# Kernel tuning notes

Measured on AMD Instinct MI355X. Metric: run time of the kernel, lower is better.

## Reference

```python
import jax, jax.numpy as jnp
import numpy as np

# Coarse-to-fine lossless 3D segmentation (Seg3dLossless), batch=1, C=1.
RES = [17, 33, 65, 129]          # odd resolutions, stride (RF-1)/(R-1) is integral
RF = RES[-1]
B_MIN, B_MAX = -1.0, 1.0
BAL = 0.5                        # balance_value
N_CONFLICT_ITERS = 2             # fixed unroll of the data-dependent while-loop


def _mlp(pts, w1, b1, w2, b2, w3, b3):
    # query_func: occupancy MLP on normalized (x,y,z) points -> [N]
    h = jax.nn.relu(pts @ w1 + b1)
    h = jax.nn.relu(h @ w2 + b2)
    return jax.nn.sigmoid(h @ w3 + b3)[..., 0]


def _eval_grid(R, w1, b1, w2, b2, w3, b3):
    # batch_eval with align_corners=False: coords2D = (coord + 0.5)/RF, mapped to [B_MIN,B_MAX]
    s = (RF - 1) // (R - 1)
    c = jnp.arange(R, dtype=jnp.float32) * s                 # final-res integer coords
    p = (c + 0.5) / RF * (B_MAX - B_MIN) + B_MIN
    zz, yy, xx = jnp.meshgrid(p, p, p, indexing='ij')        # [D,H,W]
    pts = jnp.stack([xx, yy, zz], axis=-1).reshape(-1, 3)    # (x,y,z) order
    return _mlp(pts, w1, b1, w2, b2, w3, b3).reshape(R, R, R)


def _resize(x, R):
    # trilinear, align_corners=True: out index j -> in coord j*(in-1)/(out-1)
    c = jnp.linspace(0.0, x.shape[0] - 1.0, R)
    zz, yy, xx = jnp.meshgrid(c, c, c, indexing='ij')
    return jax.scipy.ndimage.map_coordinates(x, [zz, yy, xx], order=1, mode='nearest')


def _dilate(m):
    # smooth_conv3x3 (mean filter) followed by >0 == 3x3x3 binary dilation
    f = jax.lax.reduce_window(m.astype(jnp.float32), 0.0, jax.lax.max,
                              (3, 3, 3), (1, 1, 1), 'SAME')
    return f > 0.0


def setup_inputs() -> dict:
    key = jax.random.key(0)
    k1, k2, k3 = jax.random.split(key, 3)
    H = 64
    return {
        'w1': jax.random.normal(k1, (3, H), jnp.float32) * 0.8,
        'b1': jnp.zeros((H,), jnp.float32),
        'w2': jax.random.normal(k2, (H, H), jnp.float32) * (1.0 / np.sqrt(H)),
        'b2': jnp.zeros((H,), jnp.float32),
        'w3': jax.random.normal(k3, (H, 1), jnp.float32) * (1.0 / np.sqrt(H)),
        'b3': jnp.zeros((1,), jnp.float32),
    }


def reference(w1, b1, w2, b2, w3, b3):
    params = (w1, b1, w2, b2, w3, b3)
    # level 0: dense eval on the coarse grid
    occ = _eval_grid(RES[0], *params)                        # [R0,R0,R0]
    s0 = (RF - 1) // (RES[0] - 1)
    calculated = jnp.zeros((RF, RF, RF), bool).at[::s0, ::s0, ::s0].set(True)

    for R in RES[1:]:
        s = (RF - 1) // (R - 1)
        valid = _resize((occ > BAL).astype(jnp.float32), R)  # no-grad mask path
        occ_i = _resize(occ, R)                              # differentiable interp
        boundary = _dilate((valid > 0.0) & (valid < 1.0))
        calc_l = calculated[::s, ::s, ::s]
        boundary = boundary & (~calc_l)                      # skip already-evaluated voxels
        occ_true = _eval_grid(R, *params)                    # query_func at this level
        occ = jnp.where(boundary, occ_true, occ_i)           # scatter of occupancys_topk
        calc_l = calc_l | boundary
        # conflict resolution: re-query 3^3 neighbors of sign-flip voxels
        conflict = boundary & ((occ_i - BAL) * (occ_true - BAL) < 0.0)
        for _ in range(N_CONFLICT_ITERS):
            nbr = _dilate(conflict) & (~calc_l)
            occ_prev = occ
            occ = jnp.where(nbr, occ_true, occ)
            calc_l = calc_l | nbr
            conflict = nbr & ((occ_prev - BAL) * (occ_true - BAL) < 0.0)
        calculated = calculated.at[::s, ::s, ::s].set(calc_l)

    return occ[None, None]                                   # (1, 1, D, H, W)
```

## Files before the change

### kernel.cpp

```cpp
#include <hip/hip_runtime.h>

#define HH 64

static __global__ void k_prep_w2t(const float* __restrict__ w2, float* __restrict__ w2t){
  int t = blockIdx.x * 256 + threadIdx.x;
  w2t[t] = w2[(t & 63) * HH + (t >> 6)];
}

__device__ __forceinline__ void mlp_pair(
    const float* __restrict__ sw1,
    const float* __restrict__ sw2t,
    const float* __restrict__ b2, const float* __restrict__ w3,
    const float* __restrict__ b3,
    float xA, float yA, float zA, float xB, float yB, float zB,
    float& outA, float& outB)
{
  const int ibase = ((threadIdx.x & 63) >> 5) * 32;
  float h1a[32], h1b[32];
  #pragma unroll
  for (int k = 0; k < 32; k += 4){
    const float4 wx = *(const float4*)&sw1[      ibase + k];
    const float4 wy = *(const float4*)&sw1[ 64 + ibase + k];
    const float4 wz = *(const float4*)&sw1[128 + ibase + k];
    const float4 bb = *(const float4*)&sw1[192 + ibase + k];
    h1a[k+0] = fmaxf(fmaf(xA,wx.x,fmaf(yA,wy.x,fmaf(zA,wz.x,bb.x))),0.f);
    h1a[k+1] = fmaxf(fmaf(xA,wx.y,fmaf(yA,wy.y,fmaf(zA,wz.y,bb.y))),0.f);
    h1a[k+2] = fmaxf(fmaf(xA,wx.z,fmaf(yA,wy.z,fmaf(zA,wz.z,bb.z))),0.f);
    h1a[k+3] = fmaxf(fmaf(xA,wx.w,fmaf(yA,wy.w,fmaf(zA,wz.w,bb.w))),0.f);
    h1b[k+0] = fmaxf(fmaf(xB,wx.x,fmaf(yB,wy.x,fmaf(zB,wz.x,bb.x))),0.f);
    h1b[k+1] = fmaxf(fmaf(xB,wx.y,fmaf(yB,wy.y,fmaf(zB,wz.y,bb.y))),0.f);
    h1b[k+2] = fmaxf(fmaf(xB,wx.z,fmaf(yB,wy.z,fmaf(zB,wz.z,bb.z))),0.f);
    h1b[k+3] = fmaxf(fmaf(xB,wx.w,fmaf(yB,wy.w,fmaf(zB,wz.w,bb.w))),0.f);
  }
  float oa = b3[0], ob = oa;
  #pragma unroll 1
  for (int j = 0; j < HH; ++j){
    const float4* wrow = (const float4*)&sw2t[j*HH + ibase];
    float a0 = 0.f, a1 = 0.f, c0 = 0.f, c1 = 0.f;
    #pragma unroll
    for (int q = 0; q < 8; q += 2){
      const float4 w0 = wrow[q];
      const float4 w1q = wrow[q+1];
      a0 = fmaf(h1a[4*q+0], w0.x, a0);
      a0 = fmaf(h1a[4*q+1], w0.y, a0);
      a0 = fmaf(h1a[4*q+2], w0.z, a0);
      a0 = fmaf(h1a[4*q+3], w0.w, a0);
      a1 = fmaf(h1a[4*q+4], w1q.x, a1);
      a1 = fmaf(h1a[4*q+5], w1q.y, a1);
      a1 = fmaf(h1a[4*q+6], w1q.z, a1);
      a1 = fmaf(h1a[4*q+7], w1q.w, a1);
      c0 = fmaf(h1b[4*q+0], w0.x, c0);
      c0 = fmaf(h1b[4*q+1], w0.y, c0);
      c0 = fmaf(h1b[4*q+2], w0.z, c0);
      c0 = fmaf(h1b[4*q+3], w0.w, c0);
      c1 = fmaf(h1b[4*q+4], w1q.x, c1);
      c1 = fmaf(h1b[4*q+5], w1q.y, c1);
      c1 = fmaf(h1b[4*q+6], w1q.z, c1);
      c1 = fmaf(h1b[4*q+7], w1q.w, c1);
    }
    float accA = a0 + a1, accB = c0 + c1;
    accA += __shfl_xor(accA, 32);
    accB += __shfl_xor(accB, 32);
    const float bj = b2[j], wj = w3[j];
    oa = fmaf(fmaxf(accA + bj, 0.f), wj, oa);
    ob = fmaf(fmaxf(accB + bj, 0.f), wj, ob);
  }
  outA = 1.f / (1.f + expf(-oa));
  outB = 1.f / (1.f + expf(-ob));
}

#define STAGE_WEIGHTS()                                            \
  __shared__ float sw1[4*HH];                                      \
  __shared__ float sw2t[HH*HH];                                    \
  {                                                                \
    const int t0 = threadIdx.x;                                    \
    if (t0 < 3*HH) sw1[t0] = w1[t0];                               \
    else sw1[t0] = b1[t0 - 3*HH];                                  \
    const float4* s4 = (const float4*)w2t;                         \
    float4* d4 = (float4*)sw2t;                                    \
    for (int i4 = t0; i4 < HH*HH/4; i4 += 256) d4[i4] = s4[i4];    \
    __syncthreads();                                               \
  }

static __global__ __launch_bounds__(256)
__attribute__((amdgpu_waves_per_eu(4,4)))
void k_eval_mlp(
    const float* __restrict__ w1, const float* __restrict__ b1,
    const float* __restrict__ w2t, const float* __restrict__ b2,
    const float* __restrict__ w3, const float* __restrict__ b3,
    float* __restrict__ out, unsigned char* __restrict__ calc1,
    int R, int s)
{
  STAGE_WEIGHTS();
  const unsigned int n = (unsigned int)R * (unsigned int)R * (unsigned int)R;
  const int lane = threadIdx.x & 63;
  const int wid = threadIdx.x >> 6;
  const unsigned int base = blockIdx.x * 256u + (unsigned int)(wid * 64 + (lane & 31));
  const unsigned int pidA = base < n ? base : (n - 1u);
  const unsigned int pB = base + 32u;
  const unsigned int pidB = pB < n ? pB : (n - 1u);
  const float inv129x2 = 2.0f / 129.0f;
  unsigned int cA = pidA % (unsigned int)R, rA = pidA / (unsigned int)R;
  unsigned int cB = pidB % (unsigned int)R, rB = pidB / (unsigned int)R;
  const float xA = ((float)(cA * (unsigned int)s) + 0.5f) * inv129x2 - 1.0f;
  const float yA = ((float)((rA % (unsigned int)R) * (unsigned int)s) + 0.5f) * inv129x2 - 1.0f;
  const float zA = ((float)((rA / (unsigned int)R) * (unsigned int)s) + 0.5f) * inv129x2 - 1.0f;
  const float xB = ((float)(cB * (unsigned int)s) + 0.5f) * inv129x2 - 1.0f;
  const float yB = ((float)((rB % (unsigned int)R) * (unsigned int)s) + 0.5f) * inv129x2 - 1.0f;
  const float zB = ((float)((rB / (unsigned int)R) * (unsigned int)s) + 0.5f) * inv129x2 - 1.0f;
  float oA, oB;
  mlp_pair(sw1, sw2t, b2, w3, b3, xA, yA, zA, xB, yB, zB, oA, oB);
  if ((threadIdx.x & 63) < 32){
    if (base < n){ out[pidA] = oA; if (calc1) calc1[pidA] = 1; }
    if (pB < n)  { out[pidB] = oB; if (calc1) calc1[pidB] = 1; }
  }
}

static __global__ __launch_bounds__(256)
__attribute__((amdgpu_waves_per_eu(4,4)))
void k_eval_sparse(
    const float* __restrict__ w1, const float* __restrict__ b1,
    const float* __restrict__ w2t, const float* __restrict__ b2,
    const float* __restrict__ w3, const float* __restrict__ b3,
    const int* __restrict__ idxl, const unsigned int* __restrict__ cnt,
    const float* __restrict__ occ_i,
    float* __restrict__ out, unsigned char* __restrict__ mism,
    int R, int s, unsigned int n)
{
  unsigned int count = *cnt;
  if (count > n) count = n;
  if (blockIdx.x * 256u >= count) return;
  STAGE_WEIGHTS();
  const int lane = threadIdx.x & 63;
  const int wid = threadIdx.x >> 6;
  const unsigned int slotA = blockIdx.x * 256u + (unsigned int)(wid * 64 + (lane & 31));
  const unsigned int slotB = slotA + 32u;
  const bool vA = slotA < count, vB = slotB < count;
  const unsigned int pidA = (unsigned int)idxl[vA ? slotA : 0];
  const unsigned int pidB = (unsigned int)idxl[vB ? slotB : 0];
  const float inv129x2 = 2.0f / 129.0f;
  unsigned int cA = pidA % (unsigned int)R, rA = pidA / (unsigned int)R;
  unsigned int cB = pidB % (unsigned int)R, rB = pidB / (unsigned int)R;
  const float xA = ((float)(cA * (unsigned int)s) + 0.5f) * inv129x2 - 1.0f;
  const float yA = ((float)((rA % (unsigned int)R) * (unsigned int)s) + 0.5f) * inv129x2 - 1.0f;
  const float zA = ((float)((rA / (unsigned int)R) * (unsigned int)s) + 0.5f) * inv129x2 - 1.0f;
  const float xB = ((float)(cB * (unsigned int)s) + 0.5f) * inv129x2 - 1.0f;
  const float yB = ((float)((rB % (unsigned int)R) * (unsigned int)s) + 0.5f) * inv129x2 - 1.0f;
  const float zB = ((float)((rB / (unsigned int)R) * (unsigned int)s) + 0.5f) * inv129x2 - 1.0f;
  float oA, oB;
  mlp_pair(sw1, sw2t, b2, w3, b3, xA, yA, zA, xB, yB, zB, oA, oB);
  if ((threadIdx.x & 63) < 32){
    if (vA){
      out[pidA] = oA;
      mism[pidA] = ((occ_i[pidA] - 0.5f) * (oA - 0.5f) < 0.0f) ? (unsigned char)1 : (unsigned char)0;
    }
    if (vB){
      out[pidB] = oB;
      mism[pidB] = ((occ_i[pidB] - 0.5f) * (oB - 0.5f) < 0.0f) ? (unsigned char)1 : (unsigned char)0;
    }
  }
}

static __global__ __launch_bounds__(256) void k_resize_b0(
    const float* __restrict__ prev,
    const unsigned char* __restrict__ calc_prev,
    float* __restrict__ occ_i, float* __restrict__ occ_out,
    unsigned char* __restrict__ bnd0, unsigned char* __restrict__ calc_out,
    unsigned char* __restrict__ confA, unsigned char* __restrict__ confB,
    int R, int Rp)
{
  const unsigned int n = (unsigned int)R * (unsigned int)R * (unsigned int)R;
  unsigned int gid = blockIdx.x * 256u + threadIdx.x;
  if (gid >= n) return;
  int c = (int)(gid % (unsigned int)R);
  unsigned int r = gid / (unsigned int)R;
  int b = (int)(r % (unsigned int)R);
  int a = (int)(r / (unsigned int)R);
  int a0 = a >> 1, da = a & 1;
  int b0i = b >> 1, db = b & 1;
  int c0 = c >> 1, dc = c & 1;
  float sum = 0.0f;
  int cnt = 0;
  const int tot = (da + 1) * (db + 1) * (dc + 1);
  for (int dz = 0; dz <= da; ++dz)
    for (int dy = 0; dy <= db; ++dy)
      for (int dx = 0; dx <= dc; ++dx){
        float v = prev[((unsigned int)(a0 + dz) * (unsigned int)Rp + (unsigned int)(b0i + dy)) * (unsigned int)Rp + (unsigned int)(c0 + dx)];
        sum += v;
        cnt += (v > 0.5f) ? 1 : 0;
      }
  float oi = sum / (float)tot;
  occ_i[gid] = oi;
  occ_out[gid] = oi;
  bnd0[gid] = (cnt > 0 && cnt < tot) ? 1 : 0;
  calc_out[gid] = ((da | db | dc) == 0)
      ? calc_prev[((unsigned int)a0 * (unsigned int)Rp + (unsigned int)b0i) * (unsigned int)Rp + (unsigned int)c0]
      : (unsigned char)0;
  confA[gid] = 0; confB[gid] = 0;
}

static __global__ __launch_bounds__(256) void k_resize_boundary(
    const float* __restrict__ prev, const float* __restrict__ occ_true,
    const unsigned char* __restrict__ calc_prev,
    float* __restrict__ occ_i, float* __restrict__ occ_out,
    unsigned char* __restrict__ bnd0,
    unsigned char* __restrict__ mism, unsigned char* __restrict__ calc_out,
    int R, int Rp)
{
  const unsigned int n = (unsigned int)R * (unsigned int)R * (unsigned int)R;
  unsigned int gid = blockIdx.x * 256u + threadIdx.x;
  if (gid >= n) return;
  int c = (int)(gid % (unsigned int)R);
  unsigned int r = gid / (unsigned int)R;
  int b = (int)(r % (unsigned int)R);
  int a = (int)(r / (unsigned int)R);
  int a0 = a >> 1, da = a & 1;
  int b0i = b >> 1, db = b & 1;
  int c0 = c >> 1, dc = c & 1;
  float sum = 0.0f;
  int cnt = 0;
  const int tot = (da + 1) * (db + 1) * (dc + 1);
  for (int dz = 0; dz <= da; ++dz)
    for (int dy = 0; dy <= db; ++dy)
      for (int dx = 0; dx <= dc; ++dx){
        float v = prev[((unsigned int)(a0 + dz) * (unsigned int)Rp + (unsigned int)(b0i + dy)) * (unsigned int)Rp + (unsigned int)(c0 + dx)];
        sum += v;
        cnt += (v > 0.5f) ? 1 : 0;
      }
  float oi = sum / (float)tot;
  occ_i[gid] = oi;
  occ_out[gid] = oi;
  bnd0[gid] = (cnt > 0 && cnt < tot) ? 1 : 0;
  mism[gid] = ((oi - 0.5f) * (occ_true[gid] - 0.5f) < 0.0f) ? 1 : 0;
  calc_out[gid] = ((da | db | dc) == 0)
      ? calc_prev[((unsigned int)a0 * (unsigned int)Rp + (unsigned int)b0i) * (unsigned int)Rp + (unsigned int)c0]
      : (unsigned char)0;
}

static __global__ __launch_bounds__(512) void k_dil7_tiled(
    const unsigned char* __restrict__ in, unsigned char* __restrict__ outp,
    unsigned int* __restrict__ bcnt, int R, int T)
{
  __shared__ unsigned char s0[14*14*14];
  __shared__ unsigned char s1[14*14*8];
  __shared__ unsigned char s2[14*8*8];
  __shared__ unsigned int wc[8];
  const int tile = blockIdx.x;
  const int tz = tile / (T*T);
  const int ty = (tile / T) % T;
  const int tx = tile % T;
  const int bz = tz*8 - 3, by = ty*8 - 3, bx = tx*8 - 3;
  const int t = threadIdx.x;
  for (int i = t; i < 14*14*14; i += 512){
    int lz = i / 196, rr = i % 196, ly = rr / 14, lx = rr % 14;
    int gz = bz + lz, gy = by + ly, gx = bx + lx;
    unsigned char v = 0;
    if (gz >= 0 && gz < R && gy >= 0 && gy < R && gx >= 0 && gx < R)
      v = in[((unsigned int)gz * (unsigned int)R + (unsigned int)gy) * (unsigned int)R + (unsigned int)gx];
    s0[i] = v;
  }
  __syncthreads();
  for (int i = t; i < 14*14*8; i += 512){
    int lz = i / 112, rr = i % 112, ly = rr / 8, lx = rr % 8;
    const unsigned char* p = &s0[lz*196 + ly*14 + lx];
    s1[i] = (unsigned char)(p[0]|p[1]|p[2]|p[3]|p[4]|p[5]|p[6]);
  }
  __syncthreads();
  for (int i = t; i < 14*8*8; i += 512){
    int lz = i / 64, rr = i % 64, ly = rr / 8, lx = rr % 8;
    const unsigned char* p = &s1[lz*112 + ly*8 + lx];
    s2[i] = (unsigned char)(p[0]|p[8]|p[16]|p[24]|p[32]|p[40]|p[48]);
  }
  __syncthreads();
  int lz = t >> 6, ly = (t >> 3) & 7, lx = t & 7;
  const unsigned char* p = &s2[lz*64 + ly*8 + lx];
  int m = p[0]|p[64]|p[128]|p[192]|p[256]|p[320]|p[384];
  int gz = tz*8 + lz, gy = ty*8 + ly, gx = tx*8 + lx;
  bool inb = (gz < R) && (gy < R) && (gx < R);
  if (inb) outp[((unsigned int)gz * (unsigned int)R + (unsigned int)gy) * (unsigned int)R + (unsigned int)gx]
      = (unsigned char)(m ? 1 : 0);
  unsigned long long bm = __ballot(inb && m);
  int w = t >> 6;
  if ((t & 63) == 0) wc[w] = (unsigned int)__popcll(bm);
  __syncthreads();
  if (t == 0) bcnt[blockIdx.x] = wc[0]+wc[1]+wc[2]+wc[3]+wc[4]+wc[5]+wc[6]+wc[7];
}

static __global__ __launch_bounds__(1024) void k_scan(
    unsigned int* __restrict__ bcnt, unsigned int nb, unsigned int* __restrict__ total)
{
  __shared__ unsigned int part[1024];
  const unsigned int t = threadIdx.x;
  const unsigned int chunk = (nb + 1023u) / 1024u;
  const unsigned int beg = t * chunk;
  const unsigned int end = (beg + chunk < nb) ? (beg + chunk) : nb;
  unsigned int s = 0;
  for (unsigned int i = beg; i < end; ++i) s += bcnt[i];
  part[t] = s;
  __syncthreads();
  for (int offd = 1; offd < 1024; offd <<= 1){
    unsigned int v = (t >= (unsigned int)offd) ? part[t - offd] : 0u;
    __syncthreads();
    part[t] += v;
    __syncthreads();
  }
  unsigned int run = (t == 0) ? 0u : part[t - 1];
  for (unsigned int i = beg; i < end; ++i){
    unsigned int v = bcnt[i];
    bcnt[i] = run;
    run += v;
  }
  if (t == 1023) *total = part[1023];
}

static __global__ __launch_bounds__(512) void k_scatter_tiled(
    const unsigned char* __restrict__ cand, const unsigned int* __restrict__ boff,
    int* __restrict__ idxl, int R, int T)
{
  __shared__ unsigned int wbase[8];
  const int tile = blockIdx.x;
  const int tz = tile / (T*T), ty = (tile / T) % T, tx = tile % T;
  const int t = threadIdx.x;
  int lz = t >> 6, ly = (t >> 3) & 7, lx = t & 7;
  int gz = tz*8 + lz, gy = ty*8 + ly, gx = tx*8 + lx;
  bool inb = (gz < R) && (gy < R) && (gx < R);
  int gid = inb ? (int)(((unsigned int)gz * (unsigned int)R + (unsigned int)gy) * (unsigned int)R + (unsigned int)gx) : 0;
  bool pred = inb && (cand[gid] != 0);
  unsigned long long m = __ballot(pred);
  int w = t >> 6, lane = t & 63;
  if (lane == 0) wbase[w] = (unsigned int)__popcll(m);
  __syncthreads();
  if (t == 0){
    unsigned int run = boff[blockIdx.x];
    for (int i = 0; i < 8; ++i){ unsigned int v = wbase[i]; wbase[i] = run; run += v; }
  }
  __syncthreads();
  if (pred){
    int pre = __popcll(m & ((1ull << lane) - 1ull));
    idxl[wbase[w] + (unsigned int)pre] = gid;
  }
}

static __global__ __launch_bounds__(256) void k_dilate_sparse(
    const int* __restrict__ idxl, const unsigned int* __restrict__ cnt,
    const unsigned char* __restrict__ src, const unsigned char* __restrict__ mism,
    unsigned char* __restrict__ calc, unsigned char* __restrict__ conf_out,
    int R, const float* __restrict__ occ_true, float* __restrict__ occ_out,
    unsigned int n)
{
  unsigned int count = *cnt;
  if (count > n) count = n;
  for (unsigned int slot = blockIdx.x * 256u + threadIdx.x; slot < count;
       slot += gridDim.x * 256u){
    int gid = idxl[slot];
    int c = gid % R;
    int r = gid / R;
    int b = r % R;
    int a = r / R;
    int m = 0;
    for (int dz = -1; dz <= 1; ++dz){
      int az = a + dz; if (az < 0 || az >= R) continue;
      for (int dy = -1; dy <= 1; ++dy){
        int by = b + dy; if (by < 0 || by >= R) continue;
        for (int dx = -1; dx <= 1; ++dx){
          int cx = c + dx; if (cx < 0 || cx >= R) continue;
          m |= src[(az * R + by) * R + cx];
        }
      }
    }
    unsigned char nb = (m && !calc[gid]) ? (unsigned char)1 : (unsigned char)0;
    conf_out[gid] = (nb && mism[gid]) ? (unsigned char)1 : (unsigned char)0;
    if (nb){
      calc[gid] = 1;
      occ_out[gid] = occ_true[gid];
    }
  }
}

static __global__ __launch_bounds__(512) void k_dilate3_tiled(
    const unsigned char* __restrict__ b0,
    const unsigned char* __restrict__ mism,
    unsigned char* __restrict__ calc,
    const float* __restrict__ occ_true,
    float* __restrict__ occ_out,
    int R, int T)
{
  __shared__ unsigned char sC[14*14*14];
  __shared__ unsigned char sD[14*14*14];
  __shared__ unsigned char sK[14*14*14];
  __shared__ unsigned char sM[14*14*14];
  __shared__ int s_any;
  const int tile = blockIdx.x;
  const int tz = tile / (T*T), ty = (tile / T) % T, tx = tile % T;
  const int bz = tz*8 - 3, by = ty*8 - 3, bx = tx*8 - 3;
  const int t = threadIdx.x;
  if (t == 0) s_any = 0;
  __syncthreads();
  int any = 0;
  for (int i = t; i < 2744; i += 512){
    int lz = i / 196, rr = i % 196, ly = rr / 14, lx = rr % 14;
    int gz = bz + lz, gy = by + ly, gx = bx + lx;
    bool in = (gz >= 0 && gz < R && gy >= 0 && gy < R && gx >= 0 && gx < R);
    unsigned int g = in ? (((unsigned int)gz * (unsigned int)R + (unsigned int)gy) * (unsigned int)R + (unsigned int)gx) : 0u;
    unsigned char v0 = in ? b0[g] : (unsigned char)0;
    sC[i] = v0; any |= v0;
    sK[i] = in ? calc[g] : (unsigned char)1;
    sM[i] = in ? mism[g] : (unsigned char)0;
  }
  if (any) s_any = 1;
  __syncthreads();
  if (!s_any) return;

  const int clz = 3 + (t >> 6), cly = 3 + ((t >> 3) & 7), clx = 3 + (t & 7);
  const int cp = clz*196 + cly*14 + clx;
  const unsigned char calc0 = sK[cp];
  __syncthreads();

  for (int i = t; i < 1728; i += 512){
    int lz = i / 144 + 1, rr = i % 144, ly = rr / 12 + 1, lx = rr % 12 + 1;
    int p = lz*196 + ly*14 + lx;
    int m = 0;
    #pragma unroll
    for (int dz = -1; dz <= 1; ++dz)
      #pragma unroll
      for (int dy = -1; dy <= 1; ++dy)
        #pragma unroll
        for (int dx = -1; dx <= 1; ++dx)
          m |= sC[p + dz*196 + dy*14 + dx];
    unsigned char nb = (m && !sK[p]) ? (unsigned char)1 : (unsigned char)0;
    sD[p] = (nb && sM[p]) ? (unsigned char)1 : (unsigned char)0;
    if (nb) sK[p] = 1;
  }
  __syncthreads();
  for (int i = t; i < 1000; i += 512){
    int lz = i / 100 + 2, rr = i % 100, ly = rr / 10 + 2, lx = rr % 10 + 2;
    int p = lz*196 + ly*14 + lx;
    int m = 0;
    #pragma unroll
    for (int dz = -1; dz <= 1; ++dz)
      #pragma unroll
      for (int dy = -1; dy <= 1; ++dy)
        #pragma unroll
        for (int dx = -1; dx <= 1; ++dx)
          m |= sD[p + dz*196 + dy*14 + dx];
    unsigned char nb = (m && !sK[p]) ? (unsigned char)1 : (unsigned char)0;
    sC[p] = (nb && sM[p]) ? (unsigned char)1 : (unsigned char)0;
    if (nb) sK[p] = 1;
  }
  __syncthreads();
  {
    int m = 0;
    #pragma unroll
    for (int dz = -1; dz <= 1; ++dz)
      #pragma unroll
      for (int dy = -1; dy <= 1; ++dy)
        #pragma unroll
        for (int dx = -1; dx <= 1; ++dx)
          m |= sC[cp + dz*196 + dy*14 + dx];
    if (m && !sK[cp]) sK[cp] = 1;
  }
  int gz = tz*8 + (clz - 3), gy = ty*8 + (cly - 3), gx = tx*8 + (clx - 3);
  if (gz < R && gy < R && gx < R){
    unsigned int g = ((unsigned int)gz * (unsigned int)R + (unsigned int)gy) * (unsigned int)R + (unsigned int)gx;
    unsigned char cf = sK[cp];
    calc[g] = cf;
    if (cf && !calc0) occ_out[g] = occ_true[g];
  }
}

extern "C" void kernel_launch(void* const* d_in, const int* in_sizes, int n_in,
                              void* d_out, int out_size, void* d_ws, size_t ws_size,
                              hipStream_t stream)
{
  const float* w1 = (const float*)d_in[0];
  const float* b1 = (const float*)d_in[1];
  const float* w2 = (const float*)d_in[2];
  const float* b2 = (const float*)d_in[3];
  const float* w3 = (const float*)d_in[4];
  const float* b3 = (const float*)d_in[5];
  float* out = (float*)d_out;

  const int NF = 129 * 129 * 129;
  const int NP = 65 * 65 * 65;
  char* ws = (char*)d_ws;
  size_t off = 0;
  auto alloc = [&](size_t bytes) -> void* {
    void* p = (void*)(ws + off);
    off += (bytes + 255) & ~(size_t)255;
    return p;
  };
  float* f_true  = (float*)alloc((size_t)NF * 4);
  float* f_occi  = (float*)alloc((size_t)NF * 4);
  float* f_prevA = (float*)alloc((size_t)NP * 4);
  float* f_prevB = (float*)alloc((size_t)NP * 4);
  float* f_w2t   = (float*)alloc((size_t)HH * HH * 4);
  int*   i_idx   = (int*)alloc((size_t)NF * 4);
  unsigned int* u_cnt  = (unsigned int*)alloc(256);
  unsigned int* u_bcnt = (unsigned int*)alloc(8448 * 4);
  unsigned char* b_b0    = (unsigned char*)alloc(NF);
  unsigned char* b_mism  = (unsigned char*)alloc(NF);
  unsigned char* b_confA = (unsigned char*)alloc(NF);
  unsigned char* b_confB = (unsigned char*)alloc(NF);
  unsigned char* b_calcA = (unsigned char*)alloc(NF);
  unsigned char* b_calcB = (unsigned char*)alloc(NF);
  unsigned char* b_cand  = (unsigned char*)alloc(NF);
  (void)ws_size;

  k_prep_w2t<<<16, 256, 0, stream>>>(w2, f_w2t);

  {
    int R = 17, s = 8;
    int n = R * R * R;
    int blocks = (n + 255) / 256;
    k_eval_mlp<<<blocks, 256, 0, stream>>>(w1, b1, f_w2t, b2, w3, b3, f_prevA, b_calcA, R, s);
  }

  int Rp = 17;
  float* prev = f_prevA;
  unsigned char* calcP = b_calcA;
  unsigned char* calcC = b_calcB;
  for (int li = 1; li <= 3; ++li){
    int R = 2 * Rp - 1;
    int s = 128 / (R - 1);
    unsigned int n = (unsigned int)R * (unsigned int)R * (unsigned int)R;
    int blocks = (int)((n + 255u) / 256u);
    const int T = (R + 7) / 8;
    const int tblocks = T * T * T;
    float* occ_out = (li == 3) ? out : ((prev == f_prevA) ? f_prevB : f_prevA);

    if (R == 33){
      k_eval_mlp<<<blocks, 256, 0, stream>>>(w1, b1, f_w2t, b2, w3, b3, f_true, (unsigned char*)nullptr, R, s);
      k_resize_boundary<<<blocks, 256, 0, stream>>>(prev, f_true, calcP, f_occi, occ_out, b_b0, b_mism, calcC, R, Rp);
      k_dilate3_tiled<<<tblocks, 512, 0, stream>>>(b_b0, b_mism, calcC, f_true, occ_out, R, T);
    } else {
      k_resize_b0<<<blocks, 256, 0, stream>>>(prev, calcP, f_occi, occ_out, b_b0, calcC,
                                              b_confA, b_confB, R, Rp);
      k_dil7_tiled<<<tblocks, 512, 0, stream>>>(b_b0, b_cand, u_bcnt, R, T);
      k_scan<<<1, 1024, 0, stream>>>(u_bcnt, (unsigned int)tblocks, u_cnt);
      k_scatter_tiled<<<tblocks, 512, 0, stream>>>(b_cand, u_bcnt, i_idx, R, T);
      k_eval_sparse<<<blocks, 256, 0, stream>>>(
          w1, b1, f_w2t, b2, w3, b3, i_idx, u_cnt, f_occi, f_true, b_mism, R, s, n);
      int sblocks = blocks < 4096 ? blocks : 4096;
      k_dilate_sparse<<<sblocks, 256, 0, stream>>>(i_idx, u_cnt, b_b0,    b_mism, calcC, b_confA, R, f_true, occ_out, n);
      k_dilate_sparse<<<sblocks, 256, 0, stream>>>(i_idx, u_cnt, b_confA, b_mism, calcC, b_confB, R, f_true, occ_out, n);
      k_dilate_sparse<<<sblocks, 256, 0, stream>>>(i_idx, u_cnt, b_confB, b_mism, calcC, b_confA, R, f_true, occ_out, n);
    }

    prev = occ_out;
    unsigned char* tmpc = calcP; calcP = calcC; calcC = tmpc;
    Rp = R;
  }
  (void)in_sizes; (void)n_in; (void)out_size;
}
```

Before: 308.2 us.

## Fuse dilation, compaction and sparse MLP eval into per-tile kernels

Each 8^3 tile now computes its 7x7x7 dilated candidate mask, compacts the candidates into a per-tile list in shared memory, and evaluates the MLP on them directly. This replaces the global scan, scatter and separate sparse-eval kernels. The follow-up conflict dilation kernels read per-tile lists instead of a global index list. The first two dense MLP evaluations (R=17 and R=33) are merged into one launch. The aim is fewer launches and less global traffic and serialization, at the cost of tiles with few candidates using whole blocks, per-tile weight staging, and possible load imbalance across tiles.

```diff
diff --git a/kernel.cpp b/kernel.cpp
--- a/kernel.cpp
+++ b/kernel.cpp
@@ -69,95 +69,57 @@
   outB = 1.f / (1.f + expf(-ob));
 }
 
-#define STAGE_WEIGHTS()                                            \
-  __shared__ float sw1[4*HH];                                      \
-  __shared__ float sw2t[HH*HH];                                    \
+#define STAGE_WEIGHTS(SW1, SW2T)                                   \
   {                                                                \
     const int t0 = threadIdx.x;                                    \
-    if (t0 < 3*HH) sw1[t0] = w1[t0];                               \
-    else sw1[t0] = b1[t0 - 3*HH];                                  \
+    if (t0 < 3*HH) SW1[t0] = w1[t0];                               \
+    else SW1[t0] = b1[t0 - 3*HH];                                  \
     const float4* s4 = (const float4*)w2t;                         \
-    float4* d4 = (float4*)sw2t;                                    \
+    float4* d4 = (float4*)SW2T;                                    \
     for (int i4 = t0; i4 < HH*HH/4; i4 += 256) d4[i4] = s4[i4];    \
     __syncthreads();                                               \
   }
 
+__device__ __forceinline__ void eval_point_coords(
+    unsigned int pid, int R, int s, float& x, float& y, float& z)
+{
+  const float inv129x2 = 2.0f / 129.0f;
+  unsigned int c = pid % (unsigned int)R, r = pid / (unsigned int)R;
+  x = ((float)(c * (unsigned int)s) + 0.5f) * inv129x2 - 1.0f;
+  y = ((float)((r % (unsigned int)R) * (unsigned int)s) + 0.5f) * inv129x2 - 1.0f;
+  z = ((float)((r / (unsigned int)R) * (unsigned int)s) + 0.5f) * inv129x2 - 1.0f;
+}
+
 static __global__ __launch_bounds__(256)
 __attribute__((amdgpu_waves_per_eu(4,4)))
-void k_eval_mlp(
+void k_eval_dual(
     const float* __restrict__ w1, const float* __restrict__ b1,
     const float* __restrict__ w2t, const float* __restrict__ b2,
     const float* __restrict__ w3, const float* __restrict__ b3,
-    float* __restrict__ out, unsigned char* __restrict__ calc1,
-    int R, int s)
-{
-  STAGE_WEIGHTS();
+    float* __restrict__ out17, unsigned char* __restrict__ calc17,
+    float* __restrict__ out33)
+{
+  __shared__ float sw1[4*HH];
+  __shared__ float sw2t[HH*HH];
+  STAGE_WEIGHTS(sw1, sw2t);
+  int R, s; float* outp; unsigned char* c1; unsigned int blk;
+  if (blockIdx.x < 20){ R = 17; s = 8; outp = out17; c1 = calc17; blk = blockIdx.x; }
+  else                { R = 33; s = 4; outp = out33; c1 = nullptr; blk = blockIdx.x - 20; }
   const unsigned int n = (unsigned int)R * (unsigned int)R * (unsigned int)R;
   const int lane = threadIdx.x & 63;
   const int wid = threadIdx.x >> 6;
-  const unsigned int base = blockIdx.x * 256u + (unsigned int)(wid * 64 + (lane & 31));
+  const unsigned int base = blk * 256u + (unsigned int)(wid * 64 + (lane & 31));
   const unsigned int pidA = base < n ? base : (n - 1u);
   const unsigned int pB = base + 32u;
   const unsigned int pidB = pB < n ? pB : (n - 1u);
-  const float inv129x2 = 2.0f / 129.0f;
-  unsigned int cA = pidA % (unsigned int)R, rA = pidA / (unsigned int)R;
-  unsigned int cB = pidB % (unsigned int)R, rB = pidB / (unsigned int)R;
-  const float xA = ((float)(cA * (unsigned int)s) + 0.5f) * inv129x2 - 1.0f;
-  const float yA = ((float)((rA % (unsigned int)R) * (unsigned int)s) + 0.5f) * inv129x2 - 1.0f;
-  const float zA = ((float)((rA / (unsigned int)R) * (unsigned int)s) + 0.5f) * inv129x2 - 1.0f;
-  const float xB = ((float)(cB * (unsigned int)s) + 0.5f) * inv129x2 - 1.0f;
-  const float yB = ((float)((rB % (unsigned int)R) * (unsigned int)s) + 0.5f) * inv129x2 - 1.0f;
-  const float zB = ((float)((rB / (unsigned int)R) * (unsigned int)s) + 0.5f) * inv129x2 - 1.0f;
+  float xA,yA,zA,xB,yB,zB;
+  eval_point_coords(pidA, R, s, xA, yA, zA);
+  eval_point_coords(pidB, R, s, xB, yB, zB);
   float oA, oB;
   mlp_pair(sw1, sw2t, b2, w3, b3, xA, yA, zA, xB, yB, zB, oA, oB);
-  if ((threadIdx.x & 63) < 32){
-    if (base < n){ out[pidA] = oA; if (calc1) calc1[pidA] = 1; }
-    if (pB < n)  { out[pidB] = oB; if (calc1) calc1[pidB] = 1; }
-  }
-}
-
-static __global__ __launch_bounds__(256)
-__attribute__((amdgpu_waves_per_eu(4,4)))
-void k_eval_sparse(
-    const float* __restrict__ w1, const float* __restrict__ b1,
-    const float* __restrict__ w2t, const float* __restrict__ b2,
-    const float* __restrict__ w3, const float* __restrict__ b3,
-    const int* __restrict__ idxl, const unsigned int* __restrict__ cnt,
-    const float* __restrict__ occ_i,
-    float* __restrict__ out, unsigned char* __restrict__ mism,
-    int R, int s, unsigned int n)
-{
-  unsigned int count = *cnt;
-  if (count > n) count = n;
-  if (blockIdx.x * 256u >= count) return;
-  STAGE_WEIGHTS();
-  const int lane = threadIdx.x & 63;
-  const int wid = threadIdx.x >> 6;
-  const unsigned int slotA = blockIdx.x * 256u + (unsigned int)(wid * 64 + (lane & 31));
-  const unsigned int slotB = slotA + 32u;
-  const bool vA = slotA < count, vB = slotB < count;
-  const unsigned int pidA = (unsigned int)idxl[vA ? slotA : 0];
-  const unsigned int pidB = (unsigned int)idxl[vB ? slotB : 0];
-  const float inv129x2 = 2.0f / 129.0f;
-  unsigned int cA = pidA % (unsigned int)R, rA = pidA / (unsigned int)R;
-  unsigned int cB = pidB % (unsigned int)R, rB = pidB / (unsigned int)R;
-  const float xA = ((float)(cA * (unsigned int)s) + 0.5f) * inv129x2 - 1.0f;
-  const float yA = ((float)((rA % (unsigned int)R) * (unsigned int)s) + 0.5f) * inv129x2 - 1.0f;
-  const float zA = ((float)((rA / (unsigned int)R) * (unsigned int)s) + 0.5f) * inv129x2 - 1.0f;
-  const float xB = ((float)(cB * (unsigned int)s) + 0.5f) * inv129x2 - 1.0f;
-  const float yB = ((float)((rB % (unsigned int)R) * (unsigned int)s) + 0.5f) * inv129x2 - 1.0f;
-  const float zB = ((float)((rB / (unsigned int)R) * (unsigned int)s) + 0.5f) * inv129x2 - 1.0f;
-  float oA, oB;
-  mlp_pair(sw1, sw2t, b2, w3, b3, xA, yA, zA, xB, yB, zB, oA, oB);
-  if ((threadIdx.x & 63) < 32){
-    if (vA){
-      out[pidA] = oA;
-      mism[pidA] = ((occ_i[pidA] - 0.5f) * (oA - 0.5f) < 0.0f) ? (unsigned char)1 : (unsigned char)0;
-    }
-    if (vB){
-      out[pidB] = oB;
-      mism[pidB] = ((occ_i[pidB] - 0.5f) * (oB - 0.5f) < 0.0f) ? (unsigned char)1 : (unsigned char)0;
-    }
+  if (lane < 32){
+    if (base < n){ outp[pidA] = oA; if (c1) c1[pidA] = 1; }
+    if (pB < n)  { outp[pidB] = oB; if (c1) c1[pidB] = 1; }
   }
 }
 
@@ -237,122 +199,139 @@
       : (unsigned char)0;
 }
 
-static __global__ __launch_bounds__(512) void k_dil7_tiled(
-    const unsigned char* __restrict__ in, unsigned char* __restrict__ outp,
-    unsigned int* __restrict__ bcnt, int R, int T)
+static __global__ __launch_bounds__(256)
+__attribute__((amdgpu_waves_per_eu(4,4)))
+void k_dil7_eval(
+    const float* __restrict__ w1, const float* __restrict__ b1,
+    const float* __restrict__ w2t, const float* __restrict__ b2,
+    const float* __restrict__ w3, const float* __restrict__ b3,
+    const unsigned char* __restrict__ b0,
+    const float* __restrict__ occ_i,
+    float* __restrict__ out, unsigned char* __restrict__ mism,
+    int* __restrict__ tlist, unsigned int* __restrict__ tcnt,
+    int R, int T, int s)
 {
   __shared__ unsigned char s0[14*14*14];
   __shared__ unsigned char s1[14*14*8];
   __shared__ unsigned char s2[14*8*8];
-  __shared__ unsigned int wc[8];
+  __shared__ int lidx[512];
+  __shared__ unsigned int wb[8];
+  __shared__ unsigned int lcnt;
+  __shared__ float sw1[4*HH];
+  __shared__ float sw2t[HH*HH];
+
   const int tile = blockIdx.x;
-  const int tz = tile / (T*T);
-  const int ty = (tile / T) % T;
-  const int tx = tile % T;
+  const int tz = tile / (T*T), ty = (tile / T) % T, tx = tile % T;
   const int bz = tz*8 - 3, by = ty*8 - 3, bx = tx*8 - 3;
   const int t = threadIdx.x;
-  for (int i = t; i < 14*14*14; i += 512){
+
+  for (int i = t; i < 2744; i += 256){
     int lz = i / 196, rr = i % 196, ly = rr / 14, lx = rr % 14;
     int gz = bz + lz, gy = by + ly, gx = bx + lx;
     unsigned char v = 0;
     if (gz >= 0 && gz < R && gy >= 0 && gy < R && gx >= 0 && gx < R)
-      v = in[((unsigned int)gz * (unsigned int)R + (unsigned int)gy) * (unsigned int)R + (unsigned int)gx];
+      v = b0[((unsigned int)gz * (unsigned int)R + (unsigned int)gy) * (unsigned int)R + (unsigned int)gx];
     s0[i] = v;
   }
   __syncthreads();
-  for (int i = t; i < 14*14*8; i += 512){
+  for (int i = t; i < 1568; i += 256){
     int lz = i / 112, rr = i % 112, ly = rr / 8, lx = rr % 8;
     const unsigned char* p = &s0[lz*196 + ly*14 + lx];
     s1[i] = (unsigned char)(p[0]|p[1]|p[2]|p[3]|p[4]|p[5]|p[6]);
   }
   __syncthreads();
-  for (int i = t; i < 14*8*8; i += 512){
+  for (int i = t; i < 896; i += 256){
     int lz = i / 64, rr = i % 64, ly = rr / 8, lx = rr % 8;
     const unsigned char* p = &s1[lz*112 + ly*8 + lx];
     s2[i] = (unsigned char)(p[0]|p[8]|p[16]|p[24]|p[32]|p[40]|p[48]);
   }
   __syncthreads();
-  int lz = t >> 6, ly = (t >> 3) & 7, lx = t & 7;
-  const unsigned char* p = &s2[lz*64 + ly*8 + lx];
-  int m = p[0]|p[64]|p[128]|p[192]|p[256]|p[320]|p[384];
-  int gz = tz*8 + lz, gy = ty*8 + ly, gx = tx*8 + lx;
-  bool inb = (gz < R) && (gy < R) && (gx < R);
-  if (inb) outp[((unsigned int)gz * (unsigned int)R + (unsigned int)gy) * (unsigned int)R + (unsigned int)gx]
-      = (unsigned char)(m ? 1 : 0);
-  unsigned long long bm = __ballot(inb && m);
-  int w = t >> 6;
-  if ((t & 63) == 0) wc[w] = (unsigned int)__popcll(bm);
-  __syncthreads();
-  if (t == 0) bcnt[blockIdx.x] = wc[0]+wc[1]+wc[2]+wc[3]+wc[4]+wc[5]+wc[6]+wc[7];
-}
-
-static __global__ __launch_bounds__(1024) void k_scan(
-    unsigned int* __restrict__ bcnt, unsigned int nb, unsigned int* __restrict__ total)
-{
-  __shared__ unsigned int part[1024];
-  const unsigned int t = threadIdx.x;
-  const unsigned int chunk = (nb + 1023u) / 1024u;
-  const unsigned int beg = t * chunk;
-  const unsigned int end = (beg + chunk < nb) ? (beg + chunk) : nb;
-  unsigned int s = 0;
-  for (unsigned int i = beg; i < end; ++i) s += bcnt[i];
-  part[t] = s;
-  __syncthreads();
-  for (int offd = 1; offd < 1024; offd <<= 1){
-    unsigned int v = (t >= (unsigned int)offd) ? part[t - offd] : 0u;
+  int c0i = t, c1i = t + 256;
+  int m0, m1, g0, g1;
+  bool p0, p1;
+  {
+    int lz = c0i >> 6, ly = (c0i >> 3) & 7, lx = c0i & 7;
+    const unsigned char* p = &s2[lz*64 + ly*8 + lx];
+    m0 = p[0]|p[64]|p[128]|p[192]|p[256]|p[320]|p[384];
+    int gz = tz*8 + lz, gy = ty*8 + ly, gx = tx*8 + lx;
+    bool inb = (gz < R) && (gy < R) && (gx < R);
+    g0 = inb ? (int)(((unsigned int)gz * (unsigned int)R + (unsigned int)gy) * (unsigned int)R + (unsigned int)gx) : 0;
+    p0 = inb && m0;
+  }
+  {
+    int lz = c1i >> 6, ly = (c1i >> 3) & 7, lx = c1i & 7;
+    const unsigned char* p = &s2[lz*64 + ly*8 + lx];
+    m1 = p[0]|p[64]|p[128]|p[192]|p[256]|p[320]|p[384];
+    int gz = tz*8 + lz, gy = ty*8 + ly, gx = tx*8 + lx;
+    bool inb = (gz < R) && (gy < R) && (gx < R);
+    g1 = inb ? (int)(((unsigned int)gz * (unsigned int)R + (unsigned int)gy) * (unsigned int)R + (unsigned int)gx) : 0;
+    p1 = inb && m1;
+  }
+  unsigned long long bm0 = __ballot(p0);
+  unsigned long long bm1 = __ballot(p1);
+  const int w = t >> 6, lane = t & 63;
+  if (lane == 0){ wb[w] = (unsigned int)__popcll(bm0); wb[4+w] = (unsigned int)__popcll(bm1); }
+  __syncthreads();
+  if (t == 0){
+    unsigned int run = 0;
+    for (int k = 0; k < 8; ++k){ unsigned int v = wb[k]; wb[k] = run; run += v; }
+    lcnt = run;
+    tcnt[tile] = run;
+  }
+  __syncthreads();
+  if (p0){
+    unsigned int pos = wb[w] + (unsigned int)__popcll(bm0 & ((1ull << lane) - 1ull));
+    lidx[pos] = g0; tlist[(unsigned int)tile * 512u + pos] = g0;
+  }
+  if (p1){
+    unsigned int pos = wb[4+w] + (unsigned int)__popcll(bm1 & ((1ull << lane) - 1ull));
+    lidx[pos] = g1; tlist[(unsigned int)tile * 512u + pos] = g1;
+  }
+  __syncthreads();
+  const unsigned int count = lcnt;
+  if (count == 0) return;
+
+  STAGE_WEIGHTS(sw1, sw2t);
+  const int wid = w;
+  for (unsigned int base = 0; base < count; base += 256u){
+    unsigned int slotA = base + (unsigned int)(wid * 64 + (lane & 31));
+    unsigned int slotB = slotA + 32u;
+    bool vA = slotA < count, vB = slotB < count;
+    unsigned int pidA = (unsigned int)lidx[vA ? slotA : 0];
+    unsigned int pidB = (unsigned int)lidx[vB ? slotB : 0];
+    float xA,yA,zA,xB,yB,zB;
+    eval_point_coords(pidA, R, s, xA, yA, zA);
+    eval_point_coords(pidB, R, s, xB, yB, zB);
+    float oA, oB;
+    mlp_pair(sw1, sw2t, b2, w3, b3, xA, yA, zA, xB, yB, zB, oA, oB);
+    if (lane < 32){
+      if (vA){
+        out[pidA] = oA;
+        mism[pidA] = ((occ_i[pidA] - 0.5f) * (oA - 0.5f) < 0.0f) ? (unsigned char)1 : (unsigned char)0;
+      }
+      if (vB){
+        out[pidB] = oB;
+        mism[pidB] = ((occ_i[pidB] - 0.5f) * (oB - 0.5f) < 0.0f) ? (unsigned char)1 : (unsigned char)0;
+      }
+    }
     __syncthreads();
-    part[t] += v;
-    __syncthreads();
-  }
-  unsigned int run = (t == 0) ? 0u : part[t - 1];
-  for (unsigned int i = beg; i < end; ++i){
-    unsigned int v = bcnt[i];
-    bcnt[i] = run;
-    run += v;
-  }
-  if (t == 1023) *total = part[1023];
-}
-
-static __global__ __launch_bounds__(512) void k_scatter_tiled(
-    const unsigned char* __restrict__ cand, const unsigned int* __restrict__ boff,
-    int* __restrict__ idxl, int R, int T)
-{
-  __shared__ unsigned int wbase[8];
-  const int tile = blockIdx.x;
-  const int tz = tile / (T*T), ty = (tile / T) % T, tx = tile % T;
-  const int t = threadIdx.x;
-  int lz = t >> 6, ly = (t >> 3) & 7, lx = t & 7;
-  int gz = tz*8 + lz, gy = ty*8 + ly, gx = tx*8 + lx;
-  bool inb = (gz < R) && (gy < R) && (gx < R);
-  int gid = inb ? (int)(((unsigned int)gz * (unsigned int)R + (unsigned int)gy) * (unsigned int)R + (unsigned int)gx) : 0;
-  bool pred = inb && (cand[gid] != 0);
-  unsigned long long m = __ballot(pred);
-  int w = t >> 6, lane = t & 63;
-  if (lane == 0) wbase[w] = (unsigned int)__popcll(m);
-  __syncthreads();
-  if (t == 0){
-    unsigned int run = boff[blockIdx.x];
-    for (int i = 0; i < 8; ++i){ unsigned int v = wbase[i]; wbase[i] = run; run += v; }
-  }
-  __syncthreads();
-  if (pred){
-    int pre = __popcll(m & ((1ull << lane) - 1ull));
-    idxl[wbase[w] + (unsigned int)pre] = gid;
-  }
-}
-
-static __global__ __launch_bounds__(256) void k_dilate_sparse(
-    const int* __restrict__ idxl, const unsigned int* __restrict__ cnt,
+  }
+}
+
+static __global__ __launch_bounds__(256) void k_dilate_tile(
+    const int* __restrict__ tlist, const unsigned int* __restrict__ tcnt,
     const unsigned char* __restrict__ src, const unsigned char* __restrict__ mism,
     unsigned char* __restrict__ calc, unsigned char* __restrict__ conf_out,
     int R, const float* __restrict__ occ_true, float* __restrict__ occ_out,
     unsigned int n)
 {
-  unsigned int count = *cnt;
-  if (count > n) count = n;
-  for (unsigned int slot = blockIdx.x * 256u + threadIdx.x; slot < count;
-       slot += gridDim.x * 256u){
-    int gid = idxl[slot];
+  unsigned int cnt = tcnt[blockIdx.x];
+  if (cnt > 512u) cnt = 512u;
+  if (cnt == 0) return;
+  const int* lst = &tlist[(unsigned int)blockIdx.x * 512u];
+  for (unsigned int k = threadIdx.x; k < cnt; k += 256u){
+    int gid = lst[k];
+    if ((unsigned int)gid >= n) continue;
     int c = gid % R;
     int r = gid / R;
     int b = r % R;
@@ -482,6 +461,7 @@
 
   const int NF = 129 * 129 * 129;
   const int NP = 65 * 65 * 65;
+  const int MAXTILES = 17 * 17 * 17;
   char* ws = (char*)d_ws;
   size_t off = 0;
   auto alloc = [&](size_t bytes) -> void* {
@@ -494,61 +474,59 @@
   float* f_prevA = (float*)alloc((size_t)NP * 4);
   float* f_prevB = (float*)alloc((size_t)NP * 4);
   float* f_w2t   = (float*)alloc((size_t)HH * HH * 4);
-  int*   i_idx   = (int*)alloc((size_t)NF * 4);
-  unsigned int* u_cnt  = (unsigned int*)alloc(256);
-  unsigned int* u_bcnt = (unsigned int*)alloc(8448 * 4);
+  int*   tlist   = (int*)alloc((size_t)MAXTILES * 512 * 4);
+  unsigned int* tcnt = (unsigned int*)alloc((size_t)MAXTILES * 4);
   unsigned char* b_b0    = (unsigned char*)alloc(NF);
   unsigned char* b_mism  = (unsigned char*)alloc(NF);
   unsigned char* b_confA = (unsigned char*)alloc(NF);
   unsigned char* b_confB = (unsigned char*)alloc(NF);
   unsigned char* b_calcA = (unsigned char*)alloc(NF);
   unsigned char* b_calcB = (unsigned char*)alloc(NF);
-  unsigned char* b_cand  = (unsigned char*)alloc(NF);
   (void)ws_size;
 
   k_prep_w2t<<<16, 256, 0, stream>>>(w2, f_w2t);
 
+  k_eval_dual<<<20 + 141, 256, 0, stream>>>(w1, b1, f_w2t, b2, w3, b3,
+                                            f_prevA, b_calcA, f_true);
+
   {
-    int R = 17, s = 8;
-    int n = R * R * R;
-    int blocks = (n + 255) / 256;
-    k_eval_mlp<<<blocks, 256, 0, stream>>>(w1, b1, f_w2t, b2, w3, b3, f_prevA, b_calcA, R, s);
-  }
-
-  int Rp = 17;
-  float* prev = f_prevA;
-  unsigned char* calcP = b_calcA;
-  unsigned char* calcC = b_calcB;
-  for (int li = 1; li <= 3; ++li){
-    int R = 2 * Rp - 1;
-    int s = 128 / (R - 1);
-    unsigned int n = (unsigned int)R * (unsigned int)R * (unsigned int)R;
+    int R = 33, Rp = 17;
+    unsigned int n = (unsigned int)R * R * R;
     int blocks = (int)((n + 255u) / 256u);
-    const int T = (R + 7) / 8;
-    const int tblocks = T * T * T;
-    float* occ_out = (li == 3) ? out : ((prev == f_prevA) ? f_prevB : f_prevA);
-
-    if (R == 33){
-      k_eval_mlp<<<blocks, 256, 0, stream>>>(w1, b1, f_w2t, b2, w3, b3, f_true, (unsigned char*)nullptr, R, s);
-      k_resize_boundary<<<blocks, 256, 0, stream>>>(prev, f_true, calcP, f_occi, occ_out, b_b0, b_mism, calcC, R, Rp);
-      k_dilate3_tiled<<<tblocks, 512, 0, stream>>>(b_b0, b_mism, calcC, f_true, occ_out, R, T);
-    } else {
-      k_resize_b0<<<blocks, 256, 0, stream>>>(prev, calcP, f_occi, occ_out, b_b0, calcC,
-                                              b_confA, b_confB, R, Rp);
-      k_dil7_tiled<<<tblocks, 512, 0, stream>>>(b_b0, b_cand, u_bcnt, R, T);
-      k_scan<<<1, 1024, 0, stream>>>(u_bcnt, (unsigned int)tblocks, u_cnt);
-      k_scatter_tiled<<<tblocks, 512, 0, stream>>>(b_cand, u_bcnt, i_idx, R, T);
-      k_eval_sparse<<<blocks, 256, 0, stream>>>(
-          w1, b1, f_w2t, b2, w3, b3, i_idx, u_cnt, f_occi, f_true, b_mism, R, s, n);
-      int sblocks = blocks < 4096 ? blocks : 4096;
-      k_dilate_sparse<<<sblocks, 256, 0, stream>>>(i_idx, u_cnt, b_b0,    b_mism, calcC, b_confA, R, f_true, occ_out, n);
-      k_dilate_sparse<<<sblocks, 256, 0, stream>>>(i_idx, u_cnt, b_confA, b_mism, calcC, b_confB, R, f_true, occ_out, n);
-      k_dilate_sparse<<<sblocks, 256, 0, stream>>>(i_idx, u_cnt, b_confB, b_mism, calcC, b_confA, R, f_true, occ_out, n);
-    }
-
-    prev = occ_out;
-    unsigned char* tmpc = calcP; calcP = calcC; calcC = tmpc;
-    Rp = R;
+    int T = (R + 7) / 8;
+    k_resize_boundary<<<blocks, 256, 0, stream>>>(f_prevA, f_true, b_calcA,
+        f_occi, f_prevB, b_b0, b_mism, b_calcB, R, Rp);
+    k_dilate3_tiled<<<T*T*T, 512, 0, stream>>>(b_b0, b_mism, b_calcB, f_true, f_prevB, R, T);
+  }
+
+  {
+    int R = 65, Rp = 33, s = 2;
+    unsigned int n = (unsigned int)R * R * R;
+    int blocks = (int)((n + 255u) / 256u);
+    int T = (R + 7) / 8;
+    int tb = T * T * T;
+    k_resize_b0<<<blocks, 256, 0, stream>>>(f_prevB, b_calcB, f_occi, f_prevA,
+        b_b0, b_calcA, b_confA, b_confB, R, Rp);
+    k_dil7_eval<<<tb, 256, 0, stream>>>(w1, b1, f_w2t, b2, w3, b3,
+        b_b0, f_occi, f_true, b_mism, tlist, tcnt, R, T, s);
+    k_dilate_tile<<<tb, 256, 0, stream>>>(tlist, tcnt, b_b0,    b_mism, b_calcA, b_confA, R, f_true, f_prevA, n);
+    k_dilate_tile<<<tb, 256, 0, stream>>>(tlist, tcnt, b_confA, b_mism, b_calcA, b_confB, R, f_true, f_prevA, n);
+    k_dilate_tile<<<tb, 256, 0, stream>>>(tlist, tcnt, b_confB, b_mism, b_calcA, b_confA, R, f_true, f_prevA, n);
+  }
+
+  {
+    int R = 129, Rp = 65, s = 1;
+    unsigned int n = (unsigned int)R * R * R;
+    int blocks = (int)((n + 255u) / 256u);
+    int T = (R + 7) / 8;
+    int tb = T * T * T;
+    k_resize_b0<<<blocks, 256, 0, stream>>>(f_prevA, b_calcA, f_occi, out,
+        b_b0, b_calcB, b_confA, b_confB, R, Rp);
+    k_dil7_eval<<<tb, 256, 0, stream>>>(w1, b1, f_w2t, b2, w3, b3,
+        b_b0, f_occi, f_true, b_mism, tlist, tcnt, R, T, s);
+    k_dilate_tile<<<tb, 256, 0, stream>>>(tlist, tcnt, b_b0,    b_mism, b_calcB, b_confA, R, f_true, out, n);
+    k_dilate_tile<<<tb, 256, 0, stream>>>(tlist, tcnt, b_confA, b_mism, b_calcB, b_confB, R, f_true, out, n);
+    k_dilate_tile<<<tb, 256, 0, stream>>>(tlist, tcnt, b_confB, b_mism, b_calcB, b_confA, R, f_true, out, n);
   }
   (void)in_sizes; (void)n_in; (void)out_size;
 }
```

Result: slower. 367.4 us (+19.2%).
